# Kernel tuning notes

Hardware: AMD Instinct MI355X
Metric: run time of the kernel (lower is better)

The kernel has to match this reference:

```python
import jax, jax.numpy as jnp
import numpy as np

N_NODES = 100000
N_EDGES = 1000000
IN_DIM, HID_DIM, OUT_DIM = 256, 128, 128


def setup_inputs() -> dict:
    key = jax.random.key(0)
    ks = jax.random.split(key, 6)
    return {
        "x1": jax.random.normal(ks[0], (N_NODES, IN_DIM), jnp.float32),
        "edge_index1": jax.random.randint(ks[1], (2, N_EDGES), 0, N_NODES, jnp.int64),
        "x2": jax.random.normal(ks[2], (N_NODES, IN_DIM), jnp.float32),
        "edge_index2": jax.random.randint(ks[3], (2, N_EDGES), 0, N_NODES, jnp.int64),
        "W0": jax.random.normal(ks[4], (IN_DIM, HID_DIM), jnp.float32) * (1.0 / np.sqrt(IN_DIM)),
        "b0": jnp.zeros((HID_DIM,), jnp.float32),
        "W1": jax.random.normal(ks[5], (HID_DIM, OUT_DIM), jnp.float32) * (1.0 / np.sqrt(HID_DIM)),
        "b1": jnp.zeros((OUT_DIM,), jnp.float32),
        "p1": 0,
        "p2": 0,
    }


def _gcn_backbone(x, edge_index, W0, b0, W1, b1):
    # PyG GCNConv: add self-loops, symmetric norm D^-1/2 (A+I) D^-1/2,
    # h = x @ W, aggregate src->dst, add bias.
    n = x.shape[0]
    loops = jnp.arange(n, dtype=edge_index.dtype)
    src = jnp.concatenate([edge_index[0], loops])
    dst = jnp.concatenate([edge_index[1], loops])
    deg = jax.ops.segment_sum(jnp.ones_like(dst, jnp.float32), dst, num_segments=n)
    dinv = jnp.where(deg > 0, jax.lax.rsqrt(deg), 0.0)
    coef = (dinv[src] * dinv[dst])[:, None]  # [E+n, 1]

    def conv(h, W, b):
        h = h @ W  # [n, d_out]
        return jax.ops.segment_sum(h[src] * coef, dst, num_segments=n) + b

    h = jax.nn.relu(conv(x, W0, b0))
    # dropout with p=0 / eval mode is identity
    return conv(h, W1, b1)


def _colnorm(h):
    # (h - mean(0)) / std(0), torch std is unbiased (ddof=1)
    mu = h.mean(axis=0)
    sd = h.std(axis=0, ddof=1)
    return (h - mu) / sd


def reference(x1, edge_index1, x2, edge_index2, W0, b0, W1, b1, p1, p2):
    h1 = _gcn_backbone(x1, edge_index1, W0, b0, W1, b1)
    h2 = _gcn_backbone(x2, edge_index2, W0, b0, W1, b1)
    return _colnorm(h1), _colnorm(h2)
```

## Files before the change

### kernel.cpp

```cpp
#include <hip/hip_runtime.h>

#define CDIV(a,b) (((a)+(b)-1)/(b))

typedef __bf16 bf16x8 __attribute__((ext_vector_type(8)));
typedef float  f32x4  __attribute__((ext_vector_type(4)));

__device__ __forceinline__ ushort f2bf(float f) {
    uint u = __float_as_uint(f);
    uint r = u + 0x7fffu + ((u >> 16) & 1u);
    return (ushort)(r >> 16);
}
__device__ __forceinline__ float bf_lo(uint p) { return __uint_as_float(p << 16); }
__device__ __forceinline__ float bf_hi(uint p) { return __uint_as_float(p & 0xffff0000u); }

__device__ __forceinline__ void glds16(const void* g, void* l) {
    __builtin_amdgcn_global_load_lds(
        (const __attribute__((address_space(1))) void*)g,
        (__attribute__((address_space(3))) void*)l, 16, 0, 0);
}


__global__ __launch_bounds__(256) void binA_k(const int* __restrict__ src,
                                              const int* __restrict__ dst, int E,
                                              int NB, int CAP,
                                              int* __restrict__ bcur,
                                              uint* __restrict__ binned) {
    __shared__ uint hist[512];
    __shared__ uint cur[512];
    const int t = threadIdx.x;
    for (int i = t; i < NB; i += 256) hist[i] = 0;
    __syncthreads();

    const int e0 = blockIdx.x * 4096;
    const int e1 = min(e0 + 4096, E);
    for (int e = e0 + t; e < e1; e += 256)
        atomicAdd(&hist[dst[e] >> 8], 1u);
    __syncthreads();

    for (int i = t; i < NB; i += 256) {
        uint c = hist[i];
        cur[i] = c ? (uint)atomicAdd(&bcur[i], (int)c) : 0u;
    }
    __syncthreads();

    for (int e = e0 + t; e < e1; e += 256) {
        int d = dst[e];
        int b = d >> 8;
        uint p = atomicAdd(&cur[b], 1u);
        if (p < (uint)CAP)
            binned[(size_t)b * CAP + p] = ((uint)src[e] << 8) | (uint)(d & 255);
    }
}

__global__ __launch_bounds__(256) void binB_k(const uint* __restrict__ binned,
                                              const int* __restrict__ bcur,
                                              int N, int CAP,
                                              int* __restrict__ csr,
                                              int* __restrict__ start,
                                              int* __restrict__ degc,
                                              float* __restrict__ dinv) {
    __shared__ uint hist[256];
    __shared__ uint cur[256];
    __shared__ uint wsum[4];
    const int b = blockIdx.x;
    const int t = threadIdx.x;
    int cnt = bcur[b];
    if (cnt > CAP) cnt = CAP;
    const uint* be = binned + (size_t)b * CAP;

    hist[t] = 0;
    __syncthreads();
    for (int e = t; e < cnt; e += 256) atomicAdd(&hist[be[e] & 255u], 1u);
    __syncthreads();

    uint v = hist[t];
    uint inc = v;
#pragma unroll
    for (int off = 1; off < 64; off <<= 1) {
        uint n = __shfl_up(inc, off);
        if ((t & 63) >= off) inc += n;
    }
    if ((t & 63) == 63) wsum[t >> 6] = inc;
    __syncthreads();
    uint wo = 0;
    if ((t >> 6) >= 1) wo += wsum[0];
    if ((t >> 6) >= 2) wo += wsum[1];
    if ((t >> 6) >= 3) wo += wsum[2];
    uint excl = wo + inc - v;
    cur[t] = excl;
    __syncthreads();

    const int base = b * CAP;
    for (int e = t; e < cnt; e += 256) {
        uint w = be[e];
        uint p = atomicAdd(&cur[w & 255u], 1u);
        csr[base + (int)p] = (int)(w >> 8);
    }

    int node = b * 256 + t;
    if (node < N) {
        start[node] = base + (int)excl;
        degc[node]  = (int)v;
        dinv[node]  = rsqrtf((float)(v + 1));
    }
}


__global__ __launch_bounds__(256) void pack_w_k(const float* __restrict__ W,
                                                ushort* __restrict__ Wp, int K) {
    int idx = blockIdx.x * 256 + threadIdx.x;
    int total = (K / 32) * 8 * 64;
    if (idx >= total) return;
    int l  = idx & 63;
    int nf = (idx >> 6) & 7;
    int kb = idx >> 9;
    int col = nf * 16 + (l & 15);
    int k0  = kb * 32 + (l >> 4) * 8;
    ushort o[8];
#pragma unroll
    for (int j = 0; j < 8; ++j) o[j] = f2bf(W[(size_t)(k0 + j) * 128 + col]);
    *reinterpret_cast<float4*>(Wp + (size_t)idx * 8) = *reinterpret_cast<float4*>(o);
}


template <int K, typename TIn>
__global__ __launch_bounds__(256) void gemm_mfma(const TIn* __restrict__ X,
                                                 const float4* __restrict__ Wp,
                                                 const float* __restrict__ dinv,
                                                 ushort* __restrict__ C, int N) {
    constexpr int ROWB = K * (int)sizeof(TIn);
    __shared__ char As[64 * ROWB];

    const int t    = threadIdx.x;
    const int lane = t & 63;
    const int w    = t >> 6;
    const int row0 = blockIdx.x * 64;

    if constexpr (sizeof(TIn) == 4) {
#pragma unroll
        for (int i = 0; i < 16; ++i) {
            int rr   = w * 16 + i;
            int grow = min(row0 + rr, N - 1);
            const float* src = (const float*)X + (size_t)grow * K + (size_t)(lane ^ (i & 7)) * 4;
            glds16(src, As + (size_t)rr * ROWB);
        }
    } else {
#pragma unroll
        for (int i = 0; i < 4; ++i) {
            int rr   = w * 16 + i * 4 + (lane >> 4);
            int grow = min(row0 + rr, N - 1);
            int slot = (lane & 15) ^ (rr & 7);
            const ushort* src = (const ushort*)X + (size_t)grow * K + (size_t)slot * 8;
            glds16(src, As + (size_t)(w * 16 + i * 4) * ROWB);
        }
    }
    __syncthreads();

    f32x4 acc[8] = {};
    const int r  = w * 16 + (lane & 15);
    const int kc = lane >> 4;

#pragma unroll
    for (int kb = 0; kb < K / 32; ++kb) {
        bf16x8 bfr[8];
#pragma unroll
        for (int nf = 0; nf < 8; ++nf)
            bfr[nf] = *reinterpret_cast<const bf16x8*>(Wp + (size_t)(kb * 8 + nf) * 64 + lane);

        bf16x8 a;
        if constexpr (sizeof(TIn) == 4) {
            int s0 = (kb * 8 + kc * 2) ^ (r & 7);
            int s1 = (kb * 8 + kc * 2 + 1) ^ (r & 7);
            f32x4 a0 = *reinterpret_cast<const f32x4*>(&As[(size_t)r * ROWB + (size_t)s0 * 16]);
            f32x4 a1 = *reinterpret_cast<const f32x4*>(&As[(size_t)r * ROWB + (size_t)s1 * 16]);
            a[0] = (__bf16)a0[0]; a[1] = (__bf16)a0[1]; a[2] = (__bf16)a0[2]; a[3] = (__bf16)a0[3];
            a[4] = (__bf16)a1[0]; a[5] = (__bf16)a1[1]; a[6] = (__bf16)a1[2]; a[7] = (__bf16)a1[3];
        } else {
            int s = (kb * 4 + kc) ^ (r & 7);
            a = *reinterpret_cast<const bf16x8*>(&As[(size_t)r * ROWB + (size_t)s * 16]);
        }

#pragma unroll
        for (int nf = 0; nf < 8; ++nf)
            acc[nf] = __builtin_amdgcn_mfma_f32_16x16x32_bf16(a, bfr[nf], acc[nf], 0, 0, 0);
    }

    const int rb = row0 + w * 16 + ((lane >> 4) << 2);
#pragma unroll
    for (int i = 0; i < 4; ++i) {
        int row = rb + i;
        if (row < N) {
            float dr = dinv[row];
#pragma unroll
            for (int nf = 0; nf < 8; ++nf)
                C[(size_t)row * 128 + nf * 16 + (lane & 15)] = f2bf(acc[nf][i] * dr);
        }
    }
}


template <int RELU, typename TOut>
__global__ __launch_bounds__(256) void agg_k(const ushort* __restrict__ Hin,
                                             TOut* __restrict__ Hout,
                                             const int* __restrict__ csr,
                                             const int* __restrict__ start,
                                             const int* __restrict__ degc,
                                             const float* __restrict__ dinv,
                                             const float* __restrict__ bias,
                                             int N) {
    const int wid  = threadIdx.x >> 6;
    const int lane = threadIdx.x & 63;
    const int v = blockIdx.x * 4 + wid;
    if (v >= N) return;

    float dv = dinv[v];
    int s   = start[v];
    int end = s + degc[v];

    const uint* base = reinterpret_cast<const uint*>(Hin);
    uint hp = base[(size_t)v * 64 + lane];
    float ax = bf_lo(hp);
    float ay = bf_hi(hp);

    for (int bs = s; bs < end; bs += 64) {
        int m = end - bs;
        if (m > 64) m = 64;
        int u_l = 0;
        if (lane < m) u_l = csr[bs + lane];
        int e = 0;
        for (; e + 8 <= m; e += 8) {
            uint p[8];
#pragma unroll
            for (int j = 0; j < 8; ++j) {
                int u = __shfl(u_l, e + j);
                p[j] = base[(size_t)u * 64 + lane];
            }
#pragma unroll
            for (int j = 0; j < 8; ++j) { ax += bf_lo(p[j]); ay += bf_hi(p[j]); }
        }
        if (e + 4 <= m) {
            uint p[4];
#pragma unroll
            for (int j = 0; j < 4; ++j) {
                int u = __shfl(u_l, e + j);
                p[j] = base[(size_t)u * 64 + lane];
            }
#pragma unroll
            for (int j = 0; j < 4; ++j) { ax += bf_lo(p[j]); ay += bf_hi(p[j]); }
            e += 4;
        }
        for (; e < m; ++e) {
            int u = __shfl(u_l, e);
            uint p = base[(size_t)u * 64 + lane];
            ax += bf_lo(p);
            ay += bf_hi(p);
        }
    }

    float2 b = reinterpret_cast<const float2*>(bias)[lane];
    float ox = fmaf(dv, ax, b.x);
    float oy = fmaf(dv, ay, b.y);
    if (RELU) {
        ox = fmaxf(ox, 0.f);
        oy = fmaxf(oy, 0.f);
    }
    if constexpr (sizeof(TOut) == 2) {
        uint packed = (uint)f2bf(ox) | ((uint)f2bf(oy) << 16);
        reinterpret_cast<uint*>(Hout)[(size_t)v * 64 + lane] = packed;
    } else {
        reinterpret_cast<float2*>(Hout)[(size_t)v * 64 + lane] = make_float2(ox, oy);
    }
}


__global__ __launch_bounds__(256) void colstats_k(const ushort* __restrict__ H,
                                                  float* __restrict__ stats, int N) {
    __shared__ float4 red[4][64];
    const int t  = threadIdx.x;
    const int cp = t & 63;
    const int rg = t >> 6;
    const int r0 = blockIdx.x * 512;
    const int r1 = min(r0 + 512, N);

    const uint* base = reinterpret_cast<const uint*>(H);
    float sx = 0.f, qx = 0.f, sy = 0.f, qy = 0.f;
    for (int r = r0 + rg; r < r1; r += 4) {
        uint p = base[(size_t)r * 64 + cp];
        float a = bf_lo(p), b = bf_hi(p);
        sx += a; qx = fmaf(a, a, qx);
        sy += b; qy = fmaf(b, b, qy);
    }
    red[rg][cp] = make_float4(sx, qx, sy, qy);
    __syncthreads();
    if (rg == 0) {
        float4 a0 = red[0][cp], a1 = red[1][cp], a2 = red[2][cp], a3 = red[3][cp];
        float* st = stats + (size_t)(blockIdx.x & 7) * 256;
        atomicAdd(&st[cp * 2],           a0.x + a1.x + a2.x + a3.x);
        atomicAdd(&st[cp * 2 + 1],       a0.z + a1.z + a2.z + a3.z);
        atomicAdd(&st[128 + cp * 2],     a0.y + a1.y + a2.y + a3.y);
        atomicAdd(&st[128 + cp * 2 + 1], a0.w + a1.w + a2.w + a3.w);
    }
}


__global__ __launch_bounds__(256) void colnorm_k(const ushort* __restrict__ H,
                                                 const float* __restrict__ stats,
                                                 float* __restrict__ Out, int N) {
    __shared__ float mu_s[128], rs_s[128];
    const int t = threadIdx.x;
    if (t < 128) {
        float s = 0.f, q = 0.f;
#pragma unroll
        for (int sl = 0; sl < 8; ++sl) {
            s += stats[sl * 256 + t];
            q += stats[sl * 256 + 128 + t];
        }
        float mu = s / (float)N;
        float var = (q - s * mu) / (float)(N - 1);
        mu_s[t] = mu;
        rs_s[t] = rsqrtf(var);
    }
    __syncthreads();

    size_t total = (size_t)N * 16;
    size_t stride = (size_t)gridDim.x * 256;
    for (size_t i = (size_t)blockIdx.x * 256 + t; i < total; i += stride) {
        uint4 p = reinterpret_cast<const uint4*>(H)[i];
        int c0 = ((int)(i & 15)) * 8;
        float o[8] = {bf_lo(p.x), bf_hi(p.x), bf_lo(p.y), bf_hi(p.y),
                      bf_lo(p.z), bf_hi(p.z), bf_lo(p.w), bf_hi(p.w)};
        float4 r0, r1;
        r0.x = (o[0] - mu_s[c0 + 0]) * rs_s[c0 + 0];
        r0.y = (o[1] - mu_s[c0 + 1]) * rs_s[c0 + 1];
        r0.z = (o[2] - mu_s[c0 + 2]) * rs_s[c0 + 2];
        r0.w = (o[3] - mu_s[c0 + 3]) * rs_s[c0 + 3];
        r1.x = (o[4] - mu_s[c0 + 4]) * rs_s[c0 + 4];
        r1.y = (o[5] - mu_s[c0 + 5]) * rs_s[c0 + 5];
        r1.z = (o[6] - mu_s[c0 + 6]) * rs_s[c0 + 6];
        r1.w = (o[7] - mu_s[c0 + 7]) * rs_s[c0 + 7];
        reinterpret_cast<float4*>(Out)[i * 2]     = r0;
        reinterpret_cast<float4*>(Out)[i * 2 + 1] = r1;
    }
}


extern "C" void kernel_launch(void* const* d_in, const int* in_sizes, int n_in,
                              void* d_out, int out_size, void* d_ws, size_t ws_size,
                              hipStream_t stream) {
    const float* x1  = (const float*)d_in[0];
    const int*   ei1 = (const int*)d_in[1];
    const float* x2  = (const float*)d_in[2];
    const int*   ei2 = (const int*)d_in[3];
    const float* W0  = (const float*)d_in[4];
    const float* b0  = (const float*)d_in[5];
    const float* W1  = (const float*)d_in[6];
    const float* b1  = (const float*)d_in[7];

    const int N  = in_sizes[0] / 256;
    const int E1 = in_sizes[1] / 2;
    const int E2 = in_sizes[3] / 2;
    const int Emax = E1 > E2 ? E1 : E2;

    const int NB  = CDIV(N, 256);
    int cap = (Emax / NB) * 8 / 5 + 1024;
    const int CAP = (cap + 1023) & ~1023;

    char* base = (char*)d_ws;
    size_t off = 0;
    auto carve = [&](size_t bytes) -> char* {
        char* p = base + off;
        off = (off + bytes + 255) & ~(size_t)255;
        return p;
    };
    ushort* hA    = (ushort*)carve((size_t)N * 128 * 2);
    ushort* hB    = (ushort*)carve((size_t)N * 128 * 2);
    float*  dinv  = (float*)carve((size_t)N * 4);
    int*    degc  = (int*)carve((size_t)N * 4);
    int*    startA= (int*)carve((size_t)N * 4);
    int*    csr   = (int*)carve((size_t)NB * CAP * 4);
    ushort* Wp0   = (ushort*)carve((256 / 32) * 8 * 64 * 8 * 2);
    ushort* Wp1   = (ushort*)carve((128 / 32) * 8 * 64 * 8 * 2);
    float*  stats = (float*)carve(8 * 256 * 4);
    int*    bcur  = (int*)carve((size_t)NB * 4);
    uint*   binned = (uint*)hA;

    pack_w_k<<<CDIV((256 / 32) * 8 * 64, 256), 256, 0, stream>>>(W0, Wp0, 256);
    pack_w_k<<<CDIV((128 / 32) * 8 * 64, 256), 256, 0, stream>>>(W1, Wp1, 128);

    for (int g = 0; g < 2; ++g) {
        const float* x  = g ? x2 : x1;
        const int*   ei = g ? ei2 : ei1;
        const int    E  = g ? E2 : E1;
        float* outg = (float*)d_out + (size_t)g * N * 128;

        hipMemsetAsync(bcur, 0, (size_t)NB * 4, stream);
        hipMemsetAsync(stats, 0, 8 * 256 * 4, stream);

        binA_k<<<CDIV(E, 4096), 256, 0, stream>>>(ei, ei + E, E, NB, CAP, bcur, binned);
        binB_k<<<NB, 256, 0, stream>>>(binned, bcur, N, CAP, csr, startA, degc, dinv);

        gemm_mfma<256, float><<<CDIV(N, 64), 256, 0, stream>>>(
            x, (const float4*)Wp0, dinv, hA, N);
        agg_k<1, ushort><<<CDIV(N, 4), 256, 0, stream>>>(
            hA, hB, csr, startA, degc, dinv, b0, N);

        gemm_mfma<128, ushort><<<CDIV(N, 64), 256, 0, stream>>>(
            hB, (const float4*)Wp1, dinv, hA, N);
        agg_k<0, ushort><<<CDIV(N, 4), 256, 0, stream>>>(
            hA, hB, csr, startA, degc, dinv, b1, N);

        colstats_k<<<CDIV(N, 512), 256, 0, stream>>>(hB, stats, N);
        colnorm_k<<<1024, 256, 0, stream>>>(hB, stats, outg, N);
    }
}
```

Baseline: 499.4 us.

## Batch both graphs into single launches via blockIdx.y when workspace allows

Processes the two independent GCN graphs together by adding a grid y-dimension to every kernel, with per-graph strided workspace buffers. This halves the number of kernel launches and memsets and doubles each grid, so small, latency-bound phases such as binning, colstats and colnorm fill the GPU better. It needs twice the workspace and falls back to the sequential two-pass path when the workspace is too small.

```diff
diff --git a/kernel.cpp b/kernel.cpp
--- a/kernel.cpp
+++ b/kernel.cpp
@@ -20,53 +20,67 @@
 }
 
 
-__global__ __launch_bounds__(256) void binA_k(const int* __restrict__ src,
-                                              const int* __restrict__ dst, int E,
-                                              int NB, int CAP,
-                                              int* __restrict__ bcur,
-                                              uint* __restrict__ binned) {
+__global__ __launch_bounds__(256) void binA_k(const int* __restrict__ ei0,
+                                              const int* __restrict__ ei1,
+                                              int E0, int E1, int NB, int CAP, int gbase,
+                                              int* __restrict__ bcur, int bstr,
+                                              uint* __restrict__ binned, size_t binstr) {
+    const int g = gbase + blockIdx.y;
+    const int* srcp = g ? ei1 : ei0;
+    const int  E    = g ? E1 : E0;
+    const int e0 = blockIdx.x * 4096;
+    if (e0 >= E) return;
+    const int* dstp = srcp + E;
+    int*  bc = bcur + (size_t)g * bstr;
+    uint* bn = binned + (size_t)g * binstr;
+
     __shared__ uint hist[512];
     __shared__ uint cur[512];
     const int t = threadIdx.x;
     for (int i = t; i < NB; i += 256) hist[i] = 0;
     __syncthreads();
 
-    const int e0 = blockIdx.x * 4096;
     const int e1 = min(e0 + 4096, E);
     for (int e = e0 + t; e < e1; e += 256)
-        atomicAdd(&hist[dst[e] >> 8], 1u);
+        atomicAdd(&hist[dstp[e] >> 8], 1u);
     __syncthreads();
 
     for (int i = t; i < NB; i += 256) {
         uint c = hist[i];
-        cur[i] = c ? (uint)atomicAdd(&bcur[i], (int)c) : 0u;
+        cur[i] = c ? (uint)atomicAdd(&bc[i], (int)c) : 0u;
     }
     __syncthreads();
 
     for (int e = e0 + t; e < e1; e += 256) {
-        int d = dst[e];
+        int d = dstp[e];
         int b = d >> 8;
         uint p = atomicAdd(&cur[b], 1u);
         if (p < (uint)CAP)
-            binned[(size_t)b * CAP + p] = ((uint)src[e] << 8) | (uint)(d & 255);
-    }
-}
-
-__global__ __launch_bounds__(256) void binB_k(const uint* __restrict__ binned,
-                                              const int* __restrict__ bcur,
-                                              int N, int CAP,
-                                              int* __restrict__ csr,
+            bn[(size_t)b * CAP + p] = ((uint)srcp[e] << 8) | (uint)(d & 255);
+    }
+}
+
+__global__ __launch_bounds__(256) void binB_k(const uint* __restrict__ binned, size_t binstr,
+                                              const int* __restrict__ bcur, int bstr,
+                                              int N, int CAP, int gbase,
+                                              int* __restrict__ csr, size_t cstr,
                                               int* __restrict__ start,
                                               int* __restrict__ degc,
-                                              float* __restrict__ dinv) {
+                                              float* __restrict__ dinv, int nstr) {
+    const int g = gbase + blockIdx.y;
+    const int b = blockIdx.x;
+    const int t = threadIdx.x;
+    int cnt = bcur[(size_t)g * bstr + b];
+    if (cnt > CAP) cnt = CAP;
+    const uint* be = binned + (size_t)g * binstr + (size_t)b * CAP;
+    int*   csr_g  = csr  + (size_t)g * cstr;
+    int*   st_g   = start + (size_t)g * nstr;
+    int*   dg_g   = degc  + (size_t)g * nstr;
+    float* dv_g   = dinv  + (size_t)g * nstr;
+
     __shared__ uint hist[256];
     __shared__ uint cur[256];
     __shared__ uint wsum[4];
-    const int b = blockIdx.x;
-    const int t = threadIdx.x;
-    int cnt = bcur[b];
-    if (cnt > CAP) cnt = CAP;
-    const uint* be = binned + (size_t)b * CAP;
 
     hist[t] = 0;
     __syncthreads();
@@ -94,14 +108,14 @@
     for (int e = t; e < cnt; e += 256) {
         uint w = be[e];
         uint p = atomicAdd(&cur[w & 255u], 1u);
-        csr[base + (int)p] = (int)(w >> 8);
+        csr_g[base + (int)p] = (int)(w >> 8);
     }
 
     int node = b * 256 + t;
     if (node < N) {
-        start[node] = base + (int)excl;
-        degc[node]  = (int)v;
-        dinv[node]  = rsqrtf((float)(v + 1));
+        st_g[node] = base + (int)excl;
+        dg_g[node] = (int)v;
+        dv_g[node] = rsqrtf((float)(v + 1));
     }
 }
 
@@ -124,12 +138,19 @@
 
 
 template <int K, typename TIn>
-__global__ __launch_bounds__(256) void gemm_mfma(const TIn* __restrict__ X,
+__global__ __launch_bounds__(256) void gemm_mfma(const TIn* __restrict__ X0,
+                                                 const TIn* __restrict__ X1,
                                                  const float4* __restrict__ Wp,
-                                                 const float* __restrict__ dinv,
-                                                 ushort* __restrict__ C, int N) {
+                                                 const float* __restrict__ dinv, int nstr,
+                                                 ushort* __restrict__ C, size_t hstr,
+                                                 int N, int gbase) {
     constexpr int ROWB = K * (int)sizeof(TIn);
     __shared__ char As[64 * ROWB];
+
+    const int g = gbase + blockIdx.y;
+    const TIn* X = g ? X1 : X0;
+    const float* dv = dinv + (size_t)g * nstr;
+    ushort* Cg = C + (size_t)g * hstr;
 
     const int t    = threadIdx.x;
     const int lane = t & 63;
@@ -190,34 +211,36 @@
     for (int i = 0; i < 4; ++i) {
         int row = rb + i;
         if (row < N) {
-            float dr = dinv[row];
+            float dr = dv[row];
 #pragma unroll
             for (int nf = 0; nf < 8; ++nf)
-                C[(size_t)row * 128 + nf * 16 + (lane & 15)] = f2bf(acc[nf][i] * dr);
-        }
-    }
-}
-
-
-template <int RELU, typename TOut>
-__global__ __launch_bounds__(256) void agg_k(const ushort* __restrict__ Hin,
-                                             TOut* __restrict__ Hout,
-                                             const int* __restrict__ csr,
+                Cg[(size_t)row * 128 + nf * 16 + (lane & 15)] = f2bf(acc[nf][i] * dr);
+        }
+    }
+}
+
+
+template <int RELU>
+__global__ __launch_bounds__(256) void agg_k(const ushort* __restrict__ Hin, size_t hstr,
+                                             ushort* __restrict__ Hout,
+                                             const int* __restrict__ csr, size_t cstr,
                                              const int* __restrict__ start,
                                              const int* __restrict__ degc,
-                                             const float* __restrict__ dinv,
+                                             const float* __restrict__ dinv, int nstr,
                                              const float* __restrict__ bias,
-                                             int N) {
+                                             int N, int gbase) {
+    const int g = gbase + blockIdx.y;
     const int wid  = threadIdx.x >> 6;
     const int lane = threadIdx.x & 63;
     const int v = blockIdx.x * 4 + wid;
     if (v >= N) return;
 
-    float dv = dinv[v];
-    int s   = start[v];
-    int end = s + degc[v];
-
-    const uint* base = reinterpret_cast<const uint*>(Hin);
+    const uint* base = reinterpret_cast<const uint*>(Hin + (size_t)g * hstr);
+    const int*  cs   = csr + (size_t)g * cstr;
+    float dvv = dinv[(size_t)g * nstr + v];
+    int s   = start[(size_t)g * nstr + v];
+    int end = s + degc[(size_t)g * nstr + v];
+
     uint hp = base[(size_t)v * 64 + lane];
     float ax = bf_lo(hp);
     float ay = bf_hi(hp);
@@ -226,7 +249,7 @@
         int m = end - bs;
         if (m > 64) m = 64;
         int u_l = 0;
-        if (lane < m) u_l = csr[bs + lane];
+        if (lane < m) u_l = cs[bs + lane];
         int e = 0;
         for (; e + 8 <= m; e += 8) {
             uint p[8];
@@ -258,23 +281,21 @@
     }
 
     float2 b = reinterpret_cast<const float2*>(bias)[lane];
-    float ox = fmaf(dv, ax, b.x);
-    float oy = fmaf(dv, ay, b.y);
+    float ox = fmaf(dvv, ax, b.x);
+    float oy = fmaf(dvv, ay, b.y);
     if (RELU) {
         ox = fmaxf(ox, 0.f);
         oy = fmaxf(oy, 0.f);
     }
-    if constexpr (sizeof(TOut) == 2) {
-        uint packed = (uint)f2bf(ox) | ((uint)f2bf(oy) << 16);
-        reinterpret_cast<uint*>(Hout)[(size_t)v * 64 + lane] = packed;
-    } else {
-        reinterpret_cast<float2*>(Hout)[(size_t)v * 64 + lane] = make_float2(ox, oy);
-    }
-}
-
-
-__global__ __launch_bounds__(256) void colstats_k(const ushort* __restrict__ H,
-                                                  float* __restrict__ stats, int N) {
+    uint packed = (uint)f2bf(ox) | ((uint)f2bf(oy) << 16);
+    reinterpret_cast<uint*>(Hout + (size_t)g * hstr)[(size_t)v * 64 + lane] = packed;
+}
+
+
+__global__ __launch_bounds__(256) void colstats_k(const ushort* __restrict__ H, size_t hstr,
+                                                  float* __restrict__ stats, int sstr,
+                                                  int N, int gbase) {
+    const int g = gbase + blockIdx.y;
     __shared__ float4 red[4][64];
     const int t  = threadIdx.x;
     const int cp = t & 63;
@@ -282,7 +303,7 @@
     const int r0 = blockIdx.x * 512;
     const int r1 = min(r0 + 512, N);
 
-    const uint* base = reinterpret_cast<const uint*>(H);
+    const uint* base = reinterpret_cast<const uint*>(H + (size_t)g * hstr);
     float sx = 0.f, qx = 0.f, sy = 0.f, qy = 0.f;
     for (int r = r0 + rg; r < r1; r += 4) {
         uint p = base[(size_t)r * 64 + cp];
@@ -294,7 +315,7 @@
     __syncthreads();
     if (rg == 0) {
         float4 a0 = red[0][cp], a1 = red[1][cp], a2 = red[2][cp], a3 = red[3][cp];
-        float* st = stats + (size_t)(blockIdx.x & 7) * 256;
+        float* st = stats + (size_t)g * sstr + (size_t)(blockIdx.x & 7) * 256;
         atomicAdd(&st[cp * 2],           a0.x + a1.x + a2.x + a3.x);
         atomicAdd(&st[cp * 2 + 1],       a0.z + a1.z + a2.z + a3.z);
         atomicAdd(&st[128 + cp * 2],     a0.y + a1.y + a2.y + a3.y);
@@ -303,17 +324,20 @@
 }
 
 
-__global__ __launch_bounds__(256) void colnorm_k(const ushort* __restrict__ H,
-                                                 const float* __restrict__ stats,
-                                                 float* __restrict__ Out, int N) {
+__global__ __launch_bounds__(256) void colnorm_k(const ushort* __restrict__ H, size_t hstr,
+                                                 const float* __restrict__ stats, int sstr,
+                                                 float* __restrict__ Out,
+                                                 int N, int gbase) {
+    const int g = gbase + blockIdx.y;
     __shared__ float mu_s[128], rs_s[128];
     const int t = threadIdx.x;
+    const float* st = stats + (size_t)g * sstr;
     if (t < 128) {
         float s = 0.f, q = 0.f;
 #pragma unroll
         for (int sl = 0; sl < 8; ++sl) {
-            s += stats[sl * 256 + t];
-            q += stats[sl * 256 + 128 + t];
+            s += st[sl * 256 + t];
+            q += st[sl * 256 + 128 + t];
         }
         float mu = s / (float)N;
         float var = (q - s * mu) / (float)(N - 1);
@@ -322,10 +346,12 @@
     }
     __syncthreads();
 
+    const uint4* Hb = reinterpret_cast<const uint4*>(H + (size_t)g * hstr);
+    float4* Ob = reinterpret_cast<float4*>(Out + (size_t)g * N * 128);
     size_t total = (size_t)N * 16;
     size_t stride = (size_t)gridDim.x * 256;
     for (size_t i = (size_t)blockIdx.x * 256 + t; i < total; i += stride) {
-        uint4 p = reinterpret_cast<const uint4*>(H)[i];
+        uint4 p = Hb[i];
         int c0 = ((int)(i & 15)) * 8;
         float o[8] = {bf_lo(p.x), bf_hi(p.x), bf_lo(p.y), bf_hi(p.y),
                       bf_lo(p.z), bf_hi(p.z), bf_lo(p.w), bf_hi(p.w)};
@@ -338,8 +364,8 @@
         r1.y = (o[5] - mu_s[c0 + 5]) * rs_s[c0 + 5];
         r1.z = (o[6] - mu_s[c0 + 6]) * rs_s[c0 + 6];
         r1.w = (o[7] - mu_s[c0 + 7]) * rs_s[c0 + 7];
-        reinterpret_cast<float4*>(Out)[i * 2]     = r0;
-        reinterpret_cast<float4*>(Out)[i * 2 + 1] = r1;
+        Ob[i * 2]     = r0;
+        Ob[i * 2 + 1] = r1;
     }
 }
 
@@ -361,9 +387,26 @@
     const int E2 = in_sizes[3] / 2;
     const int Emax = E1 > E2 ? E1 : E2;
 
-    const int NB  = CDIV(N, 256);
+    const int NB = CDIV(N, 256);
     int cap = (Emax / NB) * 8 / 5 + 1024;
     const int CAP = (cap + 1023) & ~1023;
+
+    size_t szH = (size_t)N * 128 * 2;
+    size_t need_merged = 2 * szH * 2
+                       + (size_t)2 * N * 4 * 3
+                       + (size_t)2 * NB * CAP * 4
+                       + 64 * 1024 + 32 * 1024
+                       + 2 * 8 * 256 * 4 + 2 * NB * 4
+                       + 16 * 256;
+    const bool merged = ws_size >= need_merged;
+    const int  G = merged ? 2 : 1;
+
+    const size_t hstr   = merged ? (size_t)N * 128 : 0;
+    const int    nstr   = merged ? N : 0;
+    const size_t cstr   = merged ? (size_t)NB * CAP : 0;
+    const int    bstr   = merged ? NB : 0;
+    const int    sstr   = merged ? 8 * 256 : 0;
+    const size_t binstr = merged ? (size_t)N * 64 : 0;
 
     char* base = (char*)d_ws;
     size_t off = 0;
@@ -372,44 +415,46 @@
         off = (off + bytes + 255) & ~(size_t)255;
         return p;
     };
-    ushort* hA    = (ushort*)carve((size_t)N * 128 * 2);
-    ushort* hB    = (ushort*)carve((size_t)N * 128 * 2);
-    float*  dinv  = (float*)carve((size_t)N * 4);
-    int*    degc  = (int*)carve((size_t)N * 4);
-    int*    startA= (int*)carve((size_t)N * 4);
-    int*    csr   = (int*)carve((size_t)NB * CAP * 4);
+    ushort* hA    = (ushort*)carve(szH * G);
+    ushort* hB    = (ushort*)carve(szH * G);
+    float*  dinv  = (float*)carve((size_t)N * 4 * G);
+    int*    degc  = (int*)carve((size_t)N * 4 * G);
+    int*    startA= (int*)carve((size_t)N * 4 * G);
+    int*    csr   = (int*)carve((size_t)NB * CAP * 4 * G);
     ushort* Wp0   = (ushort*)carve((256 / 32) * 8 * 64 * 8 * 2);
     ushort* Wp1   = (ushort*)carve((128 / 32) * 8 * 64 * 8 * 2);
-    float*  stats = (float*)carve(8 * 256 * 4);
-    int*    bcur  = (int*)carve((size_t)NB * 4);
+    float*  stats = (float*)carve(8 * 256 * 4 * G);
+    int*    bcur  = (int*)carve((size_t)NB * 4 * G);
     uint*   binned = (uint*)hA;
 
     pack_w_k<<<CDIV((256 / 32) * 8 * 64, 256), 256, 0, stream>>>(W0, Wp0, 256);
     pack_w_k<<<CDIV((128 / 32) * 8 * 64, 256), 256, 0, stream>>>(W1, Wp1, 128);
 
-    for (int g = 0; g < 2; ++g) {
-        const float* x  = g ? x2 : x1;
-        const int*   ei = g ? ei2 : ei1;
-        const int    E  = g ? E2 : E1;
-        float* outg = (float*)d_out + (size_t)g * N * 128;
-
-        hipMemsetAsync(bcur, 0, (size_t)NB * 4, stream);
-        hipMemsetAsync(stats, 0, 8 * 256 * 4, stream);
-
-        binA_k<<<CDIV(E, 4096), 256, 0, stream>>>(ei, ei + E, E, NB, CAP, bcur, binned);
-        binB_k<<<NB, 256, 0, stream>>>(binned, bcur, N, CAP, csr, startA, degc, dinv);
-
-        gemm_mfma<256, float><<<CDIV(N, 64), 256, 0, stream>>>(
-            x, (const float4*)Wp0, dinv, hA, N);
-        agg_k<1, ushort><<<CDIV(N, 4), 256, 0, stream>>>(
-            hA, hB, csr, startA, degc, dinv, b0, N);
-
-        gemm_mfma<128, ushort><<<CDIV(N, 64), 256, 0, stream>>>(
-            hB, (const float4*)Wp1, dinv, hA, N);
-        agg_k<0, ushort><<<CDIV(N, 4), 256, 0, stream>>>(
-            hA, hB, csr, startA, degc, dinv, b1, N);
-
-        colstats_k<<<CDIV(N, 512), 256, 0, stream>>>(hB, stats, N);
-        colnorm_k<<<1024, 256, 0, stream>>>(hB, stats, outg, N);
-    }
-}
+    const int npass = merged ? 1 : 2;
+    for (int pass = 0; pass < npass; ++pass) {
+        const int gbase = merged ? 0 : pass;
+
+        hipMemsetAsync(bcur, 0, (size_t)NB * 4 * G, stream);
+        hipMemsetAsync(stats, 0, 8 * 256 * 4 * G, stream);
+
+        binA_k<<<dim3(CDIV(Emax, 4096), G), 256, 0, stream>>>(
+            ei1, ei2, E1, E2, NB, CAP, gbase, bcur, bstr, binned, binstr);
+        binB_k<<<dim3(NB, G), 256, 0, stream>>>(
+            binned, binstr, bcur, bstr, N, CAP, gbase, csr, cstr, startA, degc, dinv, nstr);
+
+        gemm_mfma<256, float><<<dim3(CDIV(N, 64), G), 256, 0, stream>>>(
+            x1, x2, (const float4*)Wp0, dinv, nstr, hA, hstr, N, gbase);
+        agg_k<1><<<dim3(CDIV(N, 4), G), 256, 0, stream>>>(
+            hA, hstr, hB, csr, cstr, startA, degc, dinv, nstr, b0, N, gbase);
+
+        gemm_mfma<128, ushort><<<dim3(CDIV(N, 64), G), 256, 0, stream>>>(
+            hB, hB + hstr, (const float4*)Wp1, dinv, nstr, hA, hstr, N, gbase);
+        agg_k<0><<<dim3(CDIV(N, 4), G), 256, 0, stream>>>(
+            hA, hstr, hB, csr, cstr, startA, degc, dinv, nstr, b1, N, gbase);
+
+        colstats_k<<<dim3(CDIV(N, 512), G), 256, 0, stream>>>(
+            hB, hstr, stats, sstr, N, gbase);
+        colnorm_k<<<dim3(1024, G), 256, 0, stream>>>(
+            hB, hstr, stats, sstr, (float*)d_out, N, gbase);
+    }
+}
```

New measurement: 420.5 us (median of 2 runs). 15.8% less time.
